# Kernel optimization log

Measured on AMD Instinct MI355X. Metric: run time of the kernel, lower is better.

## Reference

```python
import jax, jax.numpy as jnp
import numpy as np
import math

V, D, NHEAD, NHID, NLAYERS = 50258, 1024, 8, 2048, 2
NUIDS, B, S, TOPK = 2000, 4, 256, 20


def layer_norm(x, g, b):
    m = x.mean(-1, keepdims=True)
    v = ((x - m) ** 2).mean(-1, keepdims=True)
    return (x - m) / jnp.sqrt(v + 1e-5) * g + b


def mha(x, Wqkv, bqkv, Wo, bo):
    Bx, Sx, Dx = x.shape
    hd = Dx // NHEAD
    qkv = x @ Wqkv.T + bqkv                       # [B,S,3D]
    q, k, v = jnp.split(qkv, 3, axis=-1)
    q = q.reshape(Bx, Sx, NHEAD, hd)
    k = k.reshape(Bx, Sx, NHEAD, hd)
    v = v.reshape(Bx, Sx, NHEAD, hd)
    att = jnp.einsum('bqhd,bkhd->bhqk', q, k) / math.sqrt(hd)
    att = jax.nn.softmax(att, axis=-1)
    o = jnp.einsum('bhqk,bkhd->bqhd', att, v).reshape(Bx, Sx, Dx)
    return o @ Wo.T + bo


def enc_layer(x, Wqkv, bqkv, Wo, bo, W1, b1, W2, b2, g1, be1, g2, be2):
    # torch TransformerEncoderLayer, post-LN, relu, dropout=0 (eval)
    x = layer_norm(x + mha(x, Wqkv, bqkv, Wo, bo), g1, be1)
    ff = jax.nn.relu(x @ W1.T + b1) @ W2.T + b2
    return layer_norm(x + ff, g2, be2)


def setup_inputs() -> dict:
    key = jax.random.key(0)
    ks = jax.random.split(key, 32)
    s = 0.02
    inp = {
        'inputs': jax.random.randint(ks[0], (B, S), 0, V),
        'uids': jnp.arange(NUIDS),
        'noise': jax.random.normal(ks[1], (NUIDS,), dtype=jnp.float32),
        'responses_hidden': jax.random.normal(ks[2], (B, S, D), dtype=jnp.float32),
        'topk': TOPK,
        'emb': jax.random.normal(ks[3], (V, D), dtype=jnp.float32) * s,
        # routing encoder (1 layer)
        'r_Wqkv': jax.random.normal(ks[4], (3 * D, D)) * s,
        'r_bqkv': jnp.zeros((3 * D,)),
        'r_Wo': jax.random.normal(ks[5], (D, D)) * s,
        'r_bo': jnp.zeros((D,)),
        'r_W1': jax.random.normal(ks[6], (NHID, D)) * s,
        'r_b1': jnp.zeros((NHID,)),
        'r_W2': jax.random.normal(ks[7], (D, NHID)) * s,
        'r_b2': jnp.zeros((D,)),
        'r_ln1g': jnp.ones((D,)), 'r_ln1b': jnp.zeros((D,)),
        'r_ln2g': jnp.ones((D,)), 'r_ln2b': jnp.zeros((D,)),
        # main encoder (NLAYERS, stacked)
        'e_Wqkv': jax.random.normal(ks[8], (NLAYERS, 3 * D, D)) * s,
        'e_bqkv': jnp.zeros((NLAYERS, 3 * D)),
        'e_Wo': jax.random.normal(ks[9], (NLAYERS, D, D)) * s,
        'e_bo': jnp.zeros((NLAYERS, D)),
        'e_W1': jax.random.normal(ks[10], (NLAYERS, NHID, D)) * s,
        'e_b1': jnp.zeros((NLAYERS, NHID)),
        'e_W2': jax.random.normal(ks[11], (NLAYERS, D, NHID)) * s,
        'e_b2': jnp.zeros((NLAYERS, D)),
        'e_ln1g': jnp.ones((NLAYERS, D)), 'e_ln1b': jnp.zeros((NLAYERS, D)),
        'e_ln2g': jnp.ones((NLAYERS, D)), 'e_ln2b': jnp.zeros((NLAYERS, D)),
        'dec_W': jax.random.normal(ks[12], (V, D)) * s,
        # 2000 tiny gates fused into one [NUIDS, D] matmul
        'gate_W': jax.random.normal(ks[13], (NUIDS, D)) * s,
        'gate_b': jnp.zeros((NUIDS,)),
    }
    return inp


def reference(inputs, uids, noise, responses_hidden, topk, emb,
              r_Wqkv, r_bqkv, r_Wo, r_bo, r_W1, r_b1, r_W2, r_b2,
              r_ln1g, r_ln1b, r_ln2g, r_ln2b,
              e_Wqkv, e_bqkv, e_Wo, e_bo, e_W1, e_b1, e_W2, e_b2,
              e_ln1g, e_ln1b, e_ln2g, e_ln2b,
              dec_W, gate_W, gate_b):
    # --- routing path ---
    h = emb[inputs]                                            # [B,S,D]
    rc = enc_layer(h, r_Wqkv, r_bqkv, r_Wo, r_bo, r_W1, r_b1,
                   r_W2, r_b2, r_ln1g, r_ln1b, r_ln2g, r_ln2b)
    rc = rc * math.sqrt(D)
    # fused per-UID gates: 2000 Linear(D,1) -> one [B,NUIDS] matmul
    rw = rc[:, -1, :] @ gate_W.T + gate_b                      # [B,NUIDS]
    bw = rw.mean(axis=0)                                       # [NUIDS]
    noisy = noise * jnp.std(bw)
    full = jnp.zeros((NUIDS,), dtype=bw.dtype).at[uids].set(bw + noisy)
    topk_w, topk_uids = jax.lax.top_k(full, topk)
    # --- target loss on joined responses ---
    x = responses_hidden
    for l in range(NLAYERS):
        x = enc_layer(x, e_Wqkv[l], e_bqkv[l], e_Wo[l], e_bo[l],
                      e_W1[l], e_b1[l], e_W2[l], e_b2[l],
                      e_ln1g[l], e_ln1b[l], e_ln2g[l], e_ln2b[l])
    logits = x @ dec_W.T                                       # [B,S,V]
    shift_logits = logits[:, :-1, :].reshape(-1, V)
    shift_labels = inputs[:, 1:].reshape(-1)
    logp = jax.nn.log_softmax(shift_logits, axis=-1)
    loss = -jnp.take_along_axis(logp, shift_labels[:, None], axis=1).mean()
    return loss, topk_w, topk_uids
```

## Files before the change

kernel.cpp:

```cpp
#include <hip/hip_runtime.h>

typedef unsigned short ushort_t;
typedef __bf16 bf16x8_t __attribute__((ext_vector_type(8)));
typedef float f32x4_t __attribute__((ext_vector_type(4)));

#define AS1(p) ((const __attribute__((address_space(1))) void*)(p))
#define AS3(p) ((__attribute__((address_space(3))) void*)(p))
#define DEVINL __device__ __forceinline__

DEVINL ushort_t f2bf(float f) {
    unsigned int u = __builtin_bit_cast(unsigned int, f);
    u += 0x7fffu + ((u >> 16) & 1u);
    return (ushort_t)(u >> 16);
}
DEVINL float bf2f(ushort_t h) {
    unsigned int u = ((unsigned int)h) << 16;
    return __builtin_bit_cast(float, u);
}

DEVINL float warp_sum(float v) {
#pragma unroll
    for (int o = 32; o > 0; o >>= 1) v += __shfl_xor(v, o);
    return v;
}
DEVINL float warp_max(float v) {
#pragma unroll
    for (int o = 32; o > 0; o >>= 1) v = fmaxf(v, __shfl_xor(v, o));
    return v;
}
DEVINL float block_sum(float v, float* sb) {
    v = warp_sum(v);
    int w = threadIdx.x >> 6;
    if ((threadIdx.x & 63) == 0) sb[w] = v;
    __syncthreads();
    v = sb[0] + sb[1] + sb[2] + sb[3];
    __syncthreads();
    return v;
}
DEVINL float block_max(float v, float* sb) {
    v = warp_max(v);
    int w = threadIdx.x >> 6;
    if ((threadIdx.x & 63) == 0) sb[w] = v;
    __syncthreads();
    v = fmaxf(fmaxf(sb[0], sb[1]), fmaxf(sb[2], sb[3]));
    __syncthreads();
    return v;
}

template <int EPI>
__global__ __launch_bounds__(256) void gemm_bt(
    const ushort_t* __restrict__ A, long lda, long sA1, long sA2,
    const ushort_t* __restrict__ B, long ldb, long sB1, long sB2,
    void* __restrict__ Cp, long ldc, long sC1, long sC2,
    const float* __restrict__ bias, int accum,
    int K, int batch2, int n_real,
    const int* __restrict__ labels,
    float* __restrict__ part_m, float* __restrict__ part_s,
    float* __restrict__ label_logit)
{
    __shared__ __align__(16) __bf16 As[128 * 32];
    __shared__ __align__(16) __bf16 Bs[128 * 32];

    const int tid = threadIdx.x;
    const int lane = tid & 63;
    const int wave = tid >> 6;
    const int wm = wave >> 1, wn = wave & 1;
    const int quad = lane >> 4, l16 = lane & 15;
    const long m0 = (long)blockIdx.y * 128;
    const long n0 = (long)blockIdx.x * 128;
    const int z = blockIdx.z;
    const int z1 = z / batch2, z2 = z % batch2;
    A += (long)z1 * sA1 + (long)z2 * sA2;
    B += (long)z1 * sB1 + (long)z2 * sB2;

    f32x4_t acc[4][4];
#pragma unroll
    for (int i = 0; i < 4; i++)
#pragma unroll
        for (int j = 0; j < 4; j++) {
            f32x4_t zv = {0.f, 0.f, 0.f, 0.f};
            acc[i][j] = zv;
        }

    const int ea = tid * 8;
    const int nkt = K >> 5;
    for (int kt = 0; kt < nkt; ++kt) {
        const int k0 = kt << 5;
#pragma unroll
        for (int inst = 0; inst < 2; ++inst) {
            int e = ea + inst * 2048;
            int row = e >> 5, kk = e & 31;
            const ushort_t* ga = A + (m0 + row) * lda + k0 + kk;
            const ushort_t* gb = B + (n0 + row) * ldb + k0 + kk;
            __builtin_amdgcn_global_load_lds(AS1(ga), AS3(As + e), 16, 0, 0);
            __builtin_amdgcn_global_load_lds(AS1(gb), AS3(Bs + e), 16, 0, 0);
        }
        __syncthreads();
        bf16x8_t af[4], bfr[4];
#pragma unroll
        for (int i = 0; i < 4; i++)
            af[i] = *(const bf16x8_t*)(As + (wm * 64 + i * 16 + l16) * 32 + quad * 8);
#pragma unroll
        for (int j = 0; j < 4; j++)
            bfr[j] = *(const bf16x8_t*)(Bs + (wn * 64 + j * 16 + l16) * 32 + quad * 8);
#pragma unroll
        for (int i = 0; i < 4; i++)
#pragma unroll
            for (int j = 0; j < 4; j++)
                acc[i][j] = __builtin_amdgcn_mfma_f32_16x16x32_bf16(af[i], bfr[j], acc[i][j], 0, 0, 0);
        __syncthreads();
    }

    if constexpr (EPI == 3) {
#pragma unroll
        for (int i = 0; i < 4; i++) {
#pragma unroll
            for (int reg = 0; reg < 4; reg++) {
                long row = m0 + wm * 64 + i * 16 + quad * 4 + reg;
                int lab = labels[row];
                float mx = -INFINITY;
#pragma unroll
                for (int j = 0; j < 4; j++) {
                    long col = n0 + wn * 64 + j * 16 + l16;
                    float v = acc[i][j][reg];
                    if (col < n_real) mx = fmaxf(mx, v);
                }
#pragma unroll
                for (int o = 8; o > 0; o >>= 1) mx = fmaxf(mx, __shfl_xor(mx, o));
                float sm = 0.f;
#pragma unroll
                for (int j = 0; j < 4; j++) {
                    long col = n0 + wn * 64 + j * 16 + l16;
                    float v = acc[i][j][reg];
                    if (col < n_real) sm += __expf(v - mx);
                    if (col == lab) label_logit[row] = v;
                }
#pragma unroll
                for (int o = 8; o > 0; o >>= 1) sm += __shfl_xor(sm, o);
                if (l16 == 0) {
                    long pidx = row * 786 + (long)blockIdx.x * 2 + wn;
                    part_m[pidx] = mx;
                    part_s[pidx] = sm;
                }
            }
        }
    } else if constexpr (EPI == 0) {
        float* C = (float*)Cp + (long)z1 * sC1 + (long)z2 * sC2;
#pragma unroll
        for (int i = 0; i < 4; i++)
#pragma unroll
            for (int reg = 0; reg < 4; reg++) {
                long row = m0 + wm * 64 + i * 16 + quad * 4 + reg;
#pragma unroll
                for (int j = 0; j < 4; j++) {
                    long col = n0 + wn * 64 + j * 16 + l16;
                    float v = acc[i][j][reg];
                    if (bias) v += bias[col];
                    long idx = row * ldc + col;
                    if (accum) v += C[idx];
                    C[idx] = v;
                }
            }
    } else {
        ushort_t* C = (ushort_t*)Cp + (long)z1 * sC1 + (long)z2 * sC2;
#pragma unroll
        for (int i = 0; i < 4; i++)
#pragma unroll
            for (int reg = 0; reg < 4; reg++) {
                long row = m0 + wm * 64 + i * 16 + quad * 4 + reg;
#pragma unroll
                for (int j = 0; j < 4; j++) {
                    long col = n0 + wn * 64 + j * 16 + l16;
                    float v = acc[i][j][reg];
                    if (bias) v += bias[col];
                    if constexpr (EPI == 2) v = fmaxf(v, 0.f);
                    C[row * ldc + col] = f2bf(v);
                }
            }
    }
}


__global__ __launch_bounds__(256) void k_convert(const float* __restrict__ src,
                                                 ushort_t* __restrict__ dst, long n) {
    long i = ((long)blockIdx.x * 256 + threadIdx.x) * 4;
    if (i >= n) return;
    float4 v = *(const float4*)(src + i);
    dst[i + 0] = f2bf(v.x); dst[i + 1] = f2bf(v.y);
    dst[i + 2] = f2bf(v.z); dst[i + 3] = f2bf(v.w);
}

__global__ __launch_bounds__(256) void k_convert_pad(const float* __restrict__ src,
                                                     ushort_t* __restrict__ dst,
                                                     long n_src, long n_dst) {
    long i = ((long)blockIdx.x * 256 + threadIdx.x) * 4;
    if (i >= n_dst) return;
    if (i < n_src) {
        float4 v = *(const float4*)(src + i);
        dst[i + 0] = f2bf(v.x); dst[i + 1] = f2bf(v.y);
        dst[i + 2] = f2bf(v.z); dst[i + 3] = f2bf(v.w);
    } else {
        dst[i + 0] = 0; dst[i + 1] = 0; dst[i + 2] = 0; dst[i + 3] = 0;
    }
}

__global__ __launch_bounds__(256) void k_convert2(const float* __restrict__ src,
                                                  ushort_t* __restrict__ hi,
                                                  ushort_t* __restrict__ lo, long n) {
    long i = ((long)blockIdx.x * 256 + threadIdx.x) * 4;
    if (i >= n) return;
    float4 v = *(const float4*)(src + i);
    float vv[4] = {v.x, v.y, v.z, v.w};
#pragma unroll
    for (int j = 0; j < 4; j++) {
        ushort_t h = f2bf(vv[j]);
        hi[i + j] = h;
        lo[i + j] = f2bf(vv[j] - bf2f(h));
    }
}

__global__ __launch_bounds__(256) void k_gather2(const int* __restrict__ inputs,
                                                 const float* __restrict__ emb,
                                                 ushort_t* __restrict__ hi,
                                                 ushort_t* __restrict__ lo) {
    int t = blockIdx.x, tid = threadIdx.x;
    long row = inputs[t];
    float4 v = *(const float4*)(emb + row * 1024 + tid * 4);
    long base = (long)t * 1024 + tid * 4;
    float vv[4] = {v.x, v.y, v.z, v.w};
#pragma unroll
    for (int j = 0; j < 4; j++) {
        ushort_t h = f2bf(vv[j]);
        hi[base + j] = h;
        lo[base + j] = f2bf(vv[j] - bf2f(h));
    }
}

__global__ __launch_bounds__(256) void k_rattn(const float* __restrict__ rqkv,
                                               float* __restrict__ o_rt) {
    int zz = blockIdx.x, b = zz >> 3, h = zz & 7, tid = threadIdx.x;
    __shared__ __align__(16) float q[128];
    __shared__ float p[256];
    __shared__ float sb[8];
    const float* base = rqkv + (long)b * 786432 + h * 128;
    if (tid < 128) q[tid] = base[(long)255 * 3072 + tid];
    __syncthreads();
    const float4* q4 = (const float4*)q;
    const float4* kr = (const float4*)(base + 1024 + (long)tid * 3072);
    float a = 0.f;
#pragma unroll 8
    for (int k = 0; k < 32; k++) {
        float4 wv = kr[k], xv = q4[k];
        a += wv.x * xv.x + wv.y * xv.y + wv.z * xv.z + wv.w * xv.w;
    }
    a *= 0.08838834764831845f;
    float m = block_max(a, sb);
    float e = __expf(a - m);
    float ssum = block_sum(e, sb);
    p[tid] = e / ssum;
    __syncthreads();
    if (tid < 128) {
        float acc = 0.f;
        const float* vb = base + 2048 + tid;
        for (int s = 0; s < 256; s++) acc += p[s] * vb[(long)s * 3072];
        o_rt[b * 1024 + h * 128 + tid] = acc;
    }
}

__global__ __launch_bounds__(256) void k_rwo(
    const float* __restrict__ o_rt, const int* __restrict__ inputs,
    const float* __restrict__ emb, const float* __restrict__ Wo,
    const float* __restrict__ bo, float* __restrict__ rbuf)
{
    __shared__ __align__(16) float xs[4096];
    int tid = threadIdx.x;
#pragma unroll
    for (int i = 0; i < 16; i++) xs[i * 256 + tid] = o_rt[i * 256 + tid];
    __syncthreads();
    int wave = tid >> 6, lane = tid & 63;
    int d = blockIdx.x * 4 + wave;
    const float4* wr = (const float4*)(Wo + (long)d * 1024) + lane * 4;
    const float4* x0 = (const float4*)xs + lane * 4;
    const float4* x1 = (const float4*)(xs + 1024) + lane * 4;
    const float4* x2 = (const float4*)(xs + 2048) + lane * 4;
    const float4* x3 = (const float4*)(xs + 3072) + lane * 4;
    float a0 = 0, a1 = 0, a2 = 0, a3 = 0;
#pragma unroll
    for (int k = 0; k < 4; k++) {
        float4 w = wr[k];
        float4 v0 = x0[k], v1 = x1[k], v2 = x2[k], v3 = x3[k];
        a0 += w.x * v0.x + w.y * v0.y + w.z * v0.z + w.w * v0.w;
        a1 += w.x * v1.x + w.y * v1.y + w.z * v1.z + w.w * v1.w;
        a2 += w.x * v2.x + w.y * v2.y + w.z * v2.z + w.w * v2.w;
        a3 += w.x * v3.x + w.y * v3.y + w.z * v3.z + w.w * v3.w;
    }
    a0 = warp_sum(a0); a1 = warp_sum(a1); a2 = warp_sum(a2); a3 = warp_sum(a3);
    if (lane < 4) {
        float a = (lane == 0) ? a0 : (lane == 1) ? a1 : (lane == 2) ? a2 : a3;
        long tok = inputs[lane * 256 + 255];
        rbuf[lane * 1024 + d] = emb[tok * 1024 + d] + bo[d] + a;
    }
}

__global__ __launch_bounds__(256) void k_rln(const float* __restrict__ r,
                                             const float* __restrict__ g,
                                             const float* __restrict__ be,
                                             float* __restrict__ outp, float scale) {
    int row = blockIdx.x, tid = threadIdx.x;
    __shared__ float sb[8];
    const float* rr = r + (long)row * 1024;
    float v[4], s = 0.f, sq = 0.f;
#pragma unroll
    for (int i = 0; i < 4; i++) {
        v[i] = rr[i * 256 + tid];
        s += v[i]; sq += v[i] * v[i];
    }
    s = block_sum(s, sb); sq = block_sum(sq, sb + 4);
    float mean = s * (1.f / 1024.f);
    float rstd = rsqrtf(sq * (1.f / 1024.f) - mean * mean + 1e-5f);
#pragma unroll
    for (int i = 0; i < 4; i++) {
        int d = i * 256 + tid;
        outp[(long)row * 1024 + d] = ((v[i] - mean) * rstd * g[d] + be[d]) * scale;
    }
}

__global__ __launch_bounds__(256) void k_rff1(
    const float* __restrict__ x1f, const float* __restrict__ W1,
    const float* __restrict__ b1, float* __restrict__ f1f)
{
    __shared__ __align__(16) float xs[4096];
    int tid = threadIdx.x;
#pragma unroll
    for (int i = 0; i < 16; i++) xs[i * 256 + tid] = x1f[i * 256 + tid];
    __syncthreads();
    int wave = tid >> 6, lane = tid & 63;
    int j = blockIdx.x * 4 + wave;
    const float4* wr = (const float4*)(W1 + (long)j * 1024) + lane * 4;
    const float4* x0 = (const float4*)xs + lane * 4;
    const float4* x1 = (const float4*)(xs + 1024) + lane * 4;
    const float4* x2 = (const float4*)(xs + 2048) + lane * 4;
    const float4* x3 = (const float4*)(xs + 3072) + lane * 4;
    float a0 = 0, a1 = 0, a2 = 0, a3 = 0;
#pragma unroll
    for (int k = 0; k < 4; k++) {
        float4 w = wr[k];
        float4 v0 = x0[k], v1 = x1[k], v2 = x2[k], v3 = x3[k];
        a0 += w.x * v0.x + w.y * v0.y + w.z * v0.z + w.w * v0.w;
        a1 += w.x * v1.x + w.y * v1.y + w.z * v1.z + w.w * v1.w;
        a2 += w.x * v2.x + w.y * v2.y + w.z * v2.z + w.w * v2.w;
        a3 += w.x * v3.x + w.y * v3.y + w.z * v3.z + w.w * v3.w;
    }
    a0 = warp_sum(a0); a1 = warp_sum(a1); a2 = warp_sum(a2); a3 = warp_sum(a3);
    if (lane < 4) {
        float a = (lane == 0) ? a0 : (lane == 1) ? a1 : (lane == 2) ? a2 : a3;
        f1f[lane * 2048 + j] = fmaxf(b1[j] + a, 0.f);
    }
}

__global__ __launch_bounds__(256) void k_rff2(
    const float* __restrict__ f1f, const float* __restrict__ x1f,
    const float* __restrict__ W2, const float* __restrict__ b2,
    float* __restrict__ r2f)
{
    __shared__ __align__(16) float xs[8192];
    int tid = threadIdx.x;
#pragma unroll
    for (int i = 0; i < 32; i++) xs[i * 256 + tid] = f1f[i * 256 + tid];
    __syncthreads();
    int wave = tid >> 6, lane = tid & 63;
    int d = blockIdx.x * 4 + wave;
    const float4* wr = (const float4*)(W2 + (long)d * 2048) + lane * 8;
    const float4* x0 = (const float4*)xs + lane * 8;
    const float4* x1 = (const float4*)(xs + 2048) + lane * 8;
    const float4* x2 = (const float4*)(xs + 4096) + lane * 8;
    const float4* x3 = (const float4*)(xs + 6144) + lane * 8;
    float a0 = 0, a1 = 0, a2 = 0, a3 = 0;
#pragma unroll
    for (int k = 0; k < 8; k++) {
        float4 w = wr[k];
        float4 v0 = x0[k], v1 = x1[k], v2 = x2[k], v3 = x3[k];
        a0 += w.x * v0.x + w.y * v0.y + w.z * v0.z + w.w * v0.w;
        a1 += w.x * v1.x + w.y * v1.y + w.z * v1.z + w.w * v1.w;
        a2 += w.x * v2.x + w.y * v2.y + w.z * v2.z + w.w * v2.w;
        a3 += w.x * v3.x + w.y * v3.y + w.z * v3.z + w.w * v3.w;
    }
    a0 = warp_sum(a0); a1 = warp_sum(a1); a2 = warp_sum(a2); a3 = warp_sum(a3);
    if (lane < 4) {
        float a = (lane == 0) ? a0 : (lane == 1) ? a1 : (lane == 2) ? a2 : a3;
        r2f[lane * 1024 + d] = x1f[lane * 1024 + d] + b2[d] + a;
    }
}

__global__ __launch_bounds__(256) void k_gate(const float* __restrict__ rc,
                                              const float* __restrict__ gw,
                                              const float* __restrict__ gb,
                                              float* __restrict__ bw) {
    __shared__ __align__(16) float xs[4096];
    int tid = threadIdx.x;
#pragma unroll
    for (int i = 0; i < 16; i++) xs[i * 256 + tid] = rc[i * 256 + tid];
    __syncthreads();
    int wave = tid >> 6, lane = tid & 63;
    int u = blockIdx.x * 4 + wave;
    const float4* wr = (const float4*)(gw + (long)u * 1024) + lane * 4;
    const float4* x0 = (const float4*)xs + lane * 4;
    const float4* x1 = (const float4*)(xs + 1024) + lane * 4;
    const float4* x2 = (const float4*)(xs + 2048) + lane * 4;
    const float4* x3 = (const float4*)(xs + 3072) + lane * 4;
    float a0 = 0, a1 = 0, a2 = 0, a3 = 0;
#pragma unroll
    for (int k = 0; k < 4; k++) {
        float4 w = wr[k];
        float4 v0 = x0[k], v1 = x1[k], v2 = x2[k], v3 = x3[k];
        a0 += w.x * v0.x + w.y * v0.y + w.z * v0.z + w.w * v0.w;
        a1 += w.x * v1.x + w.y * v1.y + w.z * v1.z + w.w * v1.w;
        a2 += w.x * v2.x + w.y * v2.y + w.z * v2.z + w.w * v2.w;
        a3 += w.x * v3.x + w.y * v3.y + w.z * v3.z + w.w * v3.w;
    }
    a0 = warp_sum(a0); a1 = warp_sum(a1); a2 = warp_sum(a2); a3 = warp_sum(a3);
    if (lane == 0)
        bw[u] = 0.25f * (a0 + a1 + a2 + a3) + gb[u];
}

__global__ __launch_bounds__(256) void k_topk(const float* __restrict__ bw,
                                              const int* __restrict__ uids,
                                              const float* __restrict__ noise,
                                              float* __restrict__ out) {
    int tid = threadIdx.x;
    __shared__ float full[2000];
    __shared__ float sb[8];
    __shared__ float rv[256];
    __shared__ int ri[256];
    float s = 0.f, sq = 0.f;
    for (int u = tid; u < 2000; u += 256) {
        float v = bw[u];
        s += v; sq += v * v;
    }
    s = block_sum(s, sb); sq = block_sum(sq, sb + 4);
    float mean = s * (1.f / 2000.f);
    float sd = sqrtf(fmaxf(sq * (1.f / 2000.f) - mean * mean, 0.f));
    for (int i = tid; i < 2000; i += 256) full[i] = 0.f;
    __syncthreads();
    for (int i = tid; i < 2000; i += 256) {
        int u = uids[i];
        if (u >= 0 && u < 2000) full[u] = bw[i] + noise[i] * sd;
    }
    __syncthreads();
    for (int it = 0; it < 20; ++it) {
        float bv = -INFINITY;
        int bi = 0x7fffffff;
        for (int i = tid; i < 2000; i += 256) {
            float v = full[i];
            if (v > bv || (v == bv && i < bi)) { bv = v; bi = i; }
        }
        rv[tid] = bv; ri[tid] = bi;
        __syncthreads();
        for (int stride = 128; stride > 0; stride >>= 1) {
            if (tid < stride) {
                float v2 = rv[tid + stride]; int i2 = ri[tid + stride];
                if (v2 > rv[tid] || (v2 == rv[tid] && i2 < ri[tid])) { rv[tid] = v2; ri[tid] = i2; }
            }
            __syncthreads();
        }
        if (tid == 0) {
            out[1 + it] = rv[0];
            out[21 + it] = (float)ri[0];
            full[ri[0]] = -INFINITY;
        }
        __syncthreads();
    }
}

__global__ __launch_bounds__(256) void k_vt(const ushort_t* __restrict__ qkv,
                                            ushort_t* __restrict__ vt) {
    int zz = blockIdx.y, b = zz >> 3, h = zz & 7;
    int s0 = blockIdx.x * 64, tid = threadIdx.x;
    __shared__ ushort_t t[64][130];
#pragma unroll
    for (int r = 0; r < 32; r++) {
        int idx = r * 256 + tid;
        int sl = idx >> 7, d = idx & 127;
        t[sl][d] = qkv[((long)(b * 256 + s0 + sl)) * 3072 + 2048 + h * 128 + d];
    }
    __syncthreads();
#pragma unroll
    for (int r = 0; r < 32; r++) {
        int idx = r * 256 + tid;
        int d = idx >> 6, sl = idx & 63;
        vt[((long)(zz * 128 + d)) * 256 + s0 + sl] = t[sl][d];
    }
}

__global__ void k_softmax(const float* __restrict__ S, ushort_t* __restrict__ P) {
    long row = blockIdx.x;
    int lane = threadIdx.x;
    const float* sr = S + row * 256;
    float v[4];
    float m = -INFINITY;
#pragma unroll
    for (int i = 0; i < 4; i++) {
        v[i] = sr[i * 64 + lane] * 0.08838834764831845f;
        m = fmaxf(m, v[i]);
    }
    m = warp_max(m);
    float s = 0.f;
#pragma unroll
    for (int i = 0; i < 4; i++) { v[i] = __expf(v[i] - m); s += v[i]; }
    s = warp_sum(s);
    float inv = 1.f / s;
#pragma unroll
    for (int i = 0; i < 4; i++) P[row * 256 + i * 64 + lane] = f2bf(v[i] * inv);
}

__global__ __launch_bounds__(256) void k_addln(const float* __restrict__ x,
                                               const float* __restrict__ y,
                                               const float* __restrict__ g,
                                               const float* __restrict__ b,
                                               float* __restrict__ xf,
                                               ushort_t* __restrict__ xb) {
    int row = blockIdx.x, tid = threadIdx.x;
    const float* xr = x + (long)row * 1024;
    const float* yr = y + (long)row * 1024;
    __shared__ float sb[8];
    float r[4], s = 0.f, sq = 0.f;
#pragma unroll
    for (int i = 0; i < 4; i++) {
        int d = i * 256 + tid;
        r[i] = xr[d] + yr[d];
        s += r[i]; sq += r[i] * r[i];
    }
    s = block_sum(s, sb); sq = block_sum(sq, sb + 4);
    float mean = s * (1.f / 1024.f);
    float rstd = rsqrtf(sq * (1.f / 1024.f) - mean * mean + 1e-5f);
#pragma unroll
    for (int i = 0; i < 4; i++) {
        int d = i * 256 + tid;
        float o = (r[i] - mean) * rstd * g[d] + b[d];
        xf[(long)row * 1024 + d] = o;
        xb[(long)row * 1024 + d] = f2bf(o);
    }
}

__global__ __launch_bounds__(256) void k_labels(const int* __restrict__ inputs,
                                                int* __restrict__ labels) {
    int t = blockIdx.x * 256 + threadIdx.x;
    labels[t] = ((t & 255) == 255) ? -1 : inputs[t + 1];
}

__global__ __launch_bounds__(256) void k_ce(const float* __restrict__ pm,
                                            const float* __restrict__ ps,
                                            const float* __restrict__ ll,
                                            const int* __restrict__ labels,
                                            float* __restrict__ rloss) {
    const int NB = 786;
    long row = blockIdx.x;
    int tid = threadIdx.x;
    __shared__ float sb[8];
    float m = -INFINITY;
    for (int i = tid; i < NB; i += 256) m = fmaxf(m, pm[row * NB + i]);
    m = block_max(m, sb);
    float s = 0.f;
    for (int i = tid; i < NB; i += 256) s += ps[row * NB + i] * __expf(pm[row * NB + i] - m);
    s = block_sum(s, sb);
    if (tid == 0) {
        int lab = labels[row];
        rloss[row] = (lab >= 0) ? (m + logf(s) - ll[row]) : 0.f;
    }
}

__global__ __launch_bounds__(256) void k_final(const float* __restrict__ rloss,
                                               float* __restrict__ out) {
    float s = 0.f;
    for (int i = threadIdx.x; i < 1024; i += 256) s += rloss[i];
    __shared__ float sb[8];
    s = block_sum(s, sb);
    if (threadIdx.x == 0) out[0] = s / 1020.0f;
}


extern "C" void kernel_launch(void* const* d_in, const int* in_sizes, int n_in,
                              void* d_out, int out_size, void* d_ws, size_t ws_size,
                              hipStream_t stream) {
    const int* inputs  = (const int*)d_in[0];
    const int* uids    = (const int*)d_in[1];
    const float* noise = (const float*)d_in[2];
    const float* resp  = (const float*)d_in[3];
    const float* emb   = (const float*)d_in[5];
    const float* r_Wqkv = (const float*)d_in[6];
    const float* r_bqkv = (const float*)d_in[7];
    const float* r_Wo = (const float*)d_in[8];
    const float* r_bo = (const float*)d_in[9];
    const float* r_W1 = (const float*)d_in[10];
    const float* r_b1 = (const float*)d_in[11];
    const float* r_W2 = (const float*)d_in[12];
    const float* r_b2 = (const float*)d_in[13];
    const float* r_ln1g = (const float*)d_in[14];
    const float* r_ln1b = (const float*)d_in[15];
    const float* r_ln2g = (const float*)d_in[16];
    const float* r_ln2b = (const float*)d_in[17];
    const float* e_Wqkv = (const float*)d_in[18];
    const float* e_bqkv = (const float*)d_in[19];
    const float* e_Wo = (const float*)d_in[20];
    const float* e_bo = (const float*)d_in[21];
    const float* e_W1 = (const float*)d_in[22];
    const float* e_b1 = (const float*)d_in[23];
    const float* e_W2 = (const float*)d_in[24];
    const float* e_b2 = (const float*)d_in[25];
    const float* e_ln1g = (const float*)d_in[26];
    const float* e_ln1b = (const float*)d_in[27];
    const float* e_ln2g = (const float*)d_in[28];
    const float* e_ln2b = (const float*)d_in[29];
    const float* dec_W = (const float*)d_in[30];
    const float* gate_W = (const float*)d_in[31];
    const float* gate_b = (const float*)d_in[32];
    float* out = (float*)d_out;
    (void)in_sizes; (void)n_in; (void)out_size; (void)ws_size;

    char* wp = (char*)d_ws;
    auto alloc = [&](size_t bytes) {
        char* p = wp;
        wp += (bytes + 255) & ~(size_t)255;
        return p;
    };
    ushort_t* wqr_hi = (ushort_t*)alloc(3145728ull * 2);
    ushort_t* wqr_lo = (ushort_t*)alloc(3145728ull * 2);
    ushort_t* wq_e = (ushort_t*)alloc(6291456ull * 2);
    ushort_t* wo_e = (ushort_t*)alloc(2097152ull * 2);
    ushort_t* w1_e = (ushort_t*)alloc(4194304ull * 2);
    ushort_t* w2_e = (ushort_t*)alloc(4194304ull * 2);
    ushort_t* decb = (ushort_t*)alloc(51511296ull * 2);
    ushort_t* h_hi = (ushort_t*)alloc(1048576ull * 2);
    ushort_t* h_lo = (ushort_t*)alloc(1048576ull * 2);
    float* rqkv = (float*)alloc(3145728ull * 4);
    float* o_rt = (float*)alloc(4096ull * 4);
    float* rbuf = (float*)alloc(4096ull * 4);
    float* x1f = (float*)alloc(4096ull * 4);
    float* f1f = (float*)alloc(8192ull * 4);
    float* r2f = (float*)alloc(4096ull * 4);
    float* rc = (float*)alloc(4096ull * 4);
    float* bw = (float*)alloc(2000ull * 4);
    ushort_t* xb = (ushort_t*)alloc(1048576ull * 2);
    float* xf = (float*)alloc(1048576ull * 4);
    ushort_t* qkvb = (ushort_t*)alloc(3145728ull * 2);
    ushort_t* vt = (ushort_t*)alloc(1048576ull * 2);
    float* Sb = (float*)alloc(2097152ull * 4);
    ushort_t* Pb = (ushort_t*)alloc(2097152ull * 2);
    ushort_t* ob = (ushort_t*)alloc(1048576ull * 2);
    float* tmpf = (float*)alloc(1048576ull * 4);
    ushort_t* ff1b = (ushort_t*)alloc(2097152ull * 2);
    float* pm = (float*)alloc(1024ull * 786 * 4);
    float* ps = (float*)alloc(1024ull * 786 * 4);
    float* ll = (float*)alloc(1024ull * 4);
    int* labels = (int*)alloc(1024ull * 4);
    float* rloss = (float*)alloc(1024ull * 4);

    auto gemm = [&](int epi, const ushort_t* A_, long lda_, long sA1_, long sA2_,
                    const ushort_t* B_, long ldb_, long sB1_, long sB2_,
                    void* C_, long ldc_, long sC1_, long sC2_,
                    const float* bias_, int accum_, int M_, int N_, int K_,
                    int batch_, int batch2_, int n_real_, const int* labels_,
                    float* pm_, float* ps_, float* ll_) {
        dim3 g((unsigned)(N_ / 128), (unsigned)(M_ / 128), (unsigned)batch_);
        switch (epi) {
        case 0: gemm_bt<0><<<g, 256, 0, stream>>>(A_, lda_, sA1_, sA2_, B_, ldb_, sB1_, sB2_, C_, ldc_, sC1_, sC2_, bias_, accum_, K_, batch2_, n_real_, labels_, pm_, ps_, ll_); break;
        case 1: gemm_bt<1><<<g, 256, 0, stream>>>(A_, lda_, sA1_, sA2_, B_, ldb_, sB1_, sB2_, C_, ldc_, sC1_, sC2_, bias_, accum_, K_, batch2_, n_real_, labels_, pm_, ps_, ll_); break;
        case 2: gemm_bt<2><<<g, 256, 0, stream>>>(A_, lda_, sA1_, sA2_, B_, ldb_, sB1_, sB2_, C_, ldc_, sC1_, sC2_, bias_, accum_, K_, batch2_, n_real_, labels_, pm_, ps_, ll_); break;
        case 3: gemm_bt<3><<<g, 256, 0, stream>>>(A_, lda_, sA1_, sA2_, B_, ldb_, sB1_, sB2_, C_, ldc_, sC1_, sC2_, bias_, accum_, K_, batch2_, n_real_, labels_, pm_, ps_, ll_); break;
        }
    };

    k_convert2<<<3072, 256, 0, stream>>>(r_Wqkv, wqr_hi, wqr_lo, 3145728L);
    k_convert<<<6144, 256, 0, stream>>>(e_Wqkv, wq_e, 6291456L);
    k_convert<<<2048, 256, 0, stream>>>(e_Wo, wo_e, 2097152L);
    k_convert<<<4096, 256, 0, stream>>>(e_W1, w1_e, 4194304L);
    k_convert<<<4096, 256, 0, stream>>>(e_W2, w2_e, 4194304L);
    k_convert_pad<<<50304, 256, 0, stream>>>(dec_W, decb, 51464192L, 51511296L);
    k_convert<<<1024, 256, 0, stream>>>(resp, xb, 1048576L);
    k_gather2<<<1024, 256, 0, stream>>>(inputs, emb, h_hi, h_lo);

    gemm(0, h_hi, 1024, 0, 0, wqr_hi, 1024, 0, 0, rqkv, 3072, 0, 0, r_bqkv, 0, 1024, 3072, 1024, 1, 1, 0, nullptr, nullptr, nullptr, nullptr);
    gemm(0, h_hi, 1024, 0, 0, wqr_lo, 1024, 0, 0, rqkv, 3072, 0, 0, nullptr, 1, 1024, 3072, 1024, 1, 1, 0, nullptr, nullptr, nullptr, nullptr);
    gemm(0, h_lo, 1024, 0, 0, wqr_hi, 1024, 0, 0, rqkv, 3072, 0, 0, nullptr, 1, 1024, 3072, 1024, 1, 1, 0, nullptr, nullptr, nullptr, nullptr);
    k_rattn<<<32, 256, 0, stream>>>(rqkv, o_rt);
    k_rwo<<<256, 256, 0, stream>>>(o_rt, inputs, emb, r_Wo, r_bo, rbuf);
    k_rln<<<4, 256, 0, stream>>>(rbuf, r_ln1g, r_ln1b, x1f, 1.0f);
    k_rff1<<<512, 256, 0, stream>>>(x1f, r_W1, r_b1, f1f);
    k_rff2<<<256, 256, 0, stream>>>(f1f, x1f, r_W2, r_b2, r2f);
    k_rln<<<4, 256, 0, stream>>>(r2f, r_ln2g, r_ln2b, rc, 32.0f);
    k_gate<<<500, 256, 0, stream>>>(rc, gate_W, gate_b, bw);
    k_topk<<<1, 256, 0, stream>>>(bw, uids, noise, out);

    for (int l = 0; l < 2; ++l) {
        gemm(1, xb, 1024, 0, 0, wq_e + (size_t)l * 3145728, 1024, 0, 0, qkvb, 3072, 0, 0,
             e_bqkv + l * 3072, 0, 1024, 3072, 1024, 1, 1, 0, nullptr, nullptr, nullptr, nullptr);
        k_vt<<<dim3(4, 32), 256, 0, stream>>>(qkvb, vt);
        gemm(0, qkvb, 3072, 786432, 128, qkvb + 1024, 3072, 786432, 128, Sb, 256, 524288, 65536,
             nullptr, 0, 256, 256, 128, 32, 8, 0, nullptr, nullptr, nullptr, nullptr);
        k_softmax<<<8192, 64, 0, stream>>>(Sb, Pb);
        gemm(1, Pb, 256, 524288, 65536, vt, 256, 262144, 32768, ob, 1024, 262144, 128,
             nullptr, 0, 256, 128, 256, 32, 8, 0, nullptr, nullptr, nullptr, nullptr);
        gemm(0, ob, 1024, 0, 0, wo_e + (size_t)l * 1048576, 1024, 0, 0, tmpf, 1024, 0, 0,
             e_bo + l * 1024, 0, 1024, 1024, 1024, 1, 1, 0, nullptr, nullptr, nullptr, nullptr);
        k_addln<<<1024, 256, 0, stream>>>((l == 0) ? resp : (const float*)xf, tmpf,
                                          e_ln1g + l * 1024, e_ln1b + l * 1024, xf, xb);
        gemm(2, xb, 1024, 0, 0, w1_e + (size_t)l * 2097152, 1024, 0, 0, ff1b, 2048, 0, 0,
             e_b1 + l * 2048, 0, 1024, 2048, 1024, 1, 1, 0, nullptr, nullptr, nullptr, nullptr);
        gemm(0, ff1b, 2048, 0, 0, w2_e + (size_t)l * 2097152, 2048, 0, 0, tmpf, 1024, 0, 0,
             e_b2 + l * 1024, 0, 1024, 1024, 2048, 1, 1, 0, nullptr, nullptr, nullptr, nullptr);
        k_addln<<<1024, 256, 0, stream>>>(xf, tmpf, e_ln2g + l * 1024, e_ln2b + l * 1024, xf, xb);
    }

    k_labels<<<4, 256, 0, stream>>>(inputs, labels);
    gemm(3, xb, 1024, 0, 0, decb, 1024, 0, 0, nullptr, 0, 0, 0,
         nullptr, 0, 1024, 50304, 1024, 1, 1, 50258, labels, pm, ps, ll);
    k_ce<<<1024, 256, 0, stream>>>(pm, ps, ll, labels, rloss);
    k_final<<<1, 256, 0, stream>>>(rloss, out);
}
```

Measured before the change: 1.345 ms.

## Fuse routing split-precision GEMMs, compute only last-token query, retile decoder CE GEMM

```diff
diff --git a/kernel.cpp b/kernel.cpp
--- a/kernel.cpp
+++ b/kernel.cpp
@@ -52,11 +52,7 @@
     const ushort_t* __restrict__ A, long lda, long sA1, long sA2,
     const ushort_t* __restrict__ B, long ldb, long sB1, long sB2,
     void* __restrict__ Cp, long ldc, long sC1, long sC2,
-    const float* __restrict__ bias, int accum,
-    int K, int batch2, int n_real,
-    const int* __restrict__ labels,
-    float* __restrict__ part_m, float* __restrict__ part_s,
-    float* __restrict__ label_logit)
+    const float* __restrict__ bias, int accum, int K, int batch2)
 {
     __shared__ __align__(16) __bf16 As[128 * 32];
     __shared__ __align__(16) __bf16 Bs[128 * 32];
@@ -90,10 +86,8 @@
         for (int inst = 0; inst < 2; ++inst) {
             int e = ea + inst * 2048;
             int row = e >> 5, kk = e & 31;
-            const ushort_t* ga = A + (m0 + row) * lda + k0 + kk;
-            const ushort_t* gb = B + (n0 + row) * ldb + k0 + kk;
-            __builtin_amdgcn_global_load_lds(AS1(ga), AS3(As + e), 16, 0, 0);
-            __builtin_amdgcn_global_load_lds(AS1(gb), AS3(Bs + e), 16, 0, 0);
+            __builtin_amdgcn_global_load_lds(AS1(A + (m0 + row) * lda + k0 + kk), AS3(As + e), 16, 0, 0);
+            __builtin_amdgcn_global_load_lds(AS1(B + (n0 + row) * ldb + k0 + kk), AS3(Bs + e), 16, 0, 0);
         }
         __syncthreads();
         bf16x8_t af[4], bfr[4];
@@ -111,40 +105,7 @@
         __syncthreads();
     }
 
-    if constexpr (EPI == 3) {
-#pragma unroll
-        for (int i = 0; i < 4; i++) {
-#pragma unroll
-            for (int reg = 0; reg < 4; reg++) {
-                long row = m0 + wm * 64 + i * 16 + quad * 4 + reg;
-                int lab = labels[row];
-                float mx = -INFINITY;
-#pragma unroll
-                for (int j = 0; j < 4; j++) {
-                    long col = n0 + wn * 64 + j * 16 + l16;
-                    float v = acc[i][j][reg];
-                    if (col < n_real) mx = fmaxf(mx, v);
-                }
-#pragma unroll
-                for (int o = 8; o > 0; o >>= 1) mx = fmaxf(mx, __shfl_xor(mx, o));
-                float sm = 0.f;
-#pragma unroll
-                for (int j = 0; j < 4; j++) {
-                    long col = n0 + wn * 64 + j * 16 + l16;
-                    float v = acc[i][j][reg];
-                    if (col < n_real) sm += __expf(v - mx);
-                    if (col == lab) label_logit[row] = v;
-                }
-#pragma unroll
-                for (int o = 8; o > 0; o >>= 1) sm += __shfl_xor(sm, o);
-                if (l16 == 0) {
-                    long pidx = row * 786 + (long)blockIdx.x * 2 + wn;
-                    part_m[pidx] = mx;
-                    part_s[pidx] = sm;
-                }
-            }
-        }
-    } else if constexpr (EPI == 0) {
+    if constexpr (EPI == 0) {
         float* C = (float*)Cp + (long)z1 * sC1 + (long)z2 * sC2;
 #pragma unroll
         for (int i = 0; i < 4; i++)
@@ -180,11 +141,190 @@
     }
 }
 
-
-__global__ __launch_bounds__(256) void k_convert(const float* __restrict__ src,
-                                                 ushort_t* __restrict__ dst, long n) {
+__global__ __launch_bounds__(256) void gemm_split(
+    const ushort_t* __restrict__ Ah, const ushort_t* __restrict__ Al, long lda,
+    const ushort_t* __restrict__ Bh, const ushort_t* __restrict__ Bl, long ldb,
+    float* __restrict__ C, long ldc, const float* __restrict__ bias, int K)
+{
+    __shared__ __align__(16) __bf16 Ahs[4096], Als[4096], Bhs[4096], Bls[4096];
+    const int tid = threadIdx.x;
+    const int lane = tid & 63;
+    const int wave = tid >> 6;
+    const int wm = wave >> 1, wn = wave & 1;
+    const int quad = lane >> 4, l16 = lane & 15;
+    const long m0 = (long)blockIdx.y * 128;
+    const long n0 = (long)blockIdx.x * 128;
+
+    f32x4_t acc[4][4];
+#pragma unroll
+    for (int i = 0; i < 4; i++)
+#pragma unroll
+        for (int j = 0; j < 4; j++) {
+            f32x4_t zv = {0.f, 0.f, 0.f, 0.f};
+            acc[i][j] = zv;
+        }
+
+    const int ea = tid * 8;
+    const int nkt = K >> 5;
+    for (int kt = 0; kt < nkt; ++kt) {
+        const int k0 = kt << 5;
+#pragma unroll
+        for (int inst = 0; inst < 2; ++inst) {
+            int e = ea + inst * 2048;
+            int row = e >> 5, kk = e & 31;
+            long ao = (m0 + row) * lda + k0 + kk;
+            long bo = (n0 + row) * ldb + k0 + kk;
+            __builtin_amdgcn_global_load_lds(AS1(Ah + ao), AS3(Ahs + e), 16, 0, 0);
+            __builtin_amdgcn_global_load_lds(AS1(Al + ao), AS3(Als + e), 16, 0, 0);
+            __builtin_amdgcn_global_load_lds(AS1(Bh + bo), AS3(Bhs + e), 16, 0, 0);
+            __builtin_amdgcn_global_load_lds(AS1(Bl + bo), AS3(Bls + e), 16, 0, 0);
+        }
+        __syncthreads();
+        bf16x8_t ah[4], al[4], bh[4], bl[4];
+#pragma unroll
+        for (int i = 0; i < 4; i++) {
+            int off = (wm * 64 + i * 16 + l16) * 32 + quad * 8;
+            ah[i] = *(const bf16x8_t*)(Ahs + off);
+            al[i] = *(const bf16x8_t*)(Als + off);
+        }
+#pragma unroll
+        for (int j = 0; j < 4; j++) {
+            int off = (wn * 64 + j * 16 + l16) * 32 + quad * 8;
+            bh[j] = *(const bf16x8_t*)(Bhs + off);
+            bl[j] = *(const bf16x8_t*)(Bls + off);
+        }
+#pragma unroll
+        for (int i = 0; i < 4; i++)
+#pragma unroll
+            for (int j = 0; j < 4; j++) {
+                acc[i][j] = __builtin_amdgcn_mfma_f32_16x16x32_bf16(al[i], bh[j], acc[i][j], 0, 0, 0);
+                acc[i][j] = __builtin_amdgcn_mfma_f32_16x16x32_bf16(ah[i], bl[j], acc[i][j], 0, 0, 0);
+                acc[i][j] = __builtin_amdgcn_mfma_f32_16x16x32_bf16(ah[i], bh[j], acc[i][j], 0, 0, 0);
+            }
+        __syncthreads();
+    }
+
+#pragma unroll
+    for (int i = 0; i < 4; i++)
+#pragma unroll
+        for (int reg = 0; reg < 4; reg++) {
+            long row = m0 + wm * 64 + i * 16 + quad * 4 + reg;
+#pragma unroll
+            for (int j = 0; j < 4; j++) {
+                long col = n0 + wn * 64 + j * 16 + l16;
+                C[row * ldc + col] = acc[i][j][reg] + bias[col];
+            }
+        }
+}
+
+__global__ __launch_bounds__(256) void gemm_ce(
+    const ushort_t* __restrict__ A, long lda,
+    const ushort_t* __restrict__ B, long ldb,
+    int K, int n_real, const int* __restrict__ inputs,
+    float* __restrict__ part_m, float* __restrict__ part_s,
+    float* __restrict__ label_logit)
+{
+    __shared__ __align__(16) __bf16 As[256 * 32];
+    __shared__ __align__(16) __bf16 Bs[128 * 32];
+
+    const int tid = threadIdx.x;
+    const int lane = tid & 63;
+    const int wave = tid >> 6;
+    const int quad = lane >> 4, l16 = lane & 15;
+    const long m0 = (long)blockIdx.y * 256;
+    const long n0 = (long)blockIdx.x * 128;
+
+    f32x4_t acc[4][8];
+#pragma unroll
+    for (int i = 0; i < 4; i++)
+#pragma unroll
+        for (int j = 0; j < 8; j++) {
+            f32x4_t zv = {0.f, 0.f, 0.f, 0.f};
+            acc[i][j] = zv;
+        }
+
+    const int ea = tid * 8;
+    const int nkt = K >> 5;
+    for (int kt = 0; kt < nkt; ++kt) {
+        const int k0 = kt << 5;
+#pragma unroll
+        for (int inst = 0; inst < 4; ++inst) {
+            int e = ea + inst * 2048;
+            int row = e >> 5, kk = e & 31;
+            __builtin_amdgcn_global_load_lds(AS1(A + (m0 + row) * lda + k0 + kk), AS3(As + e), 16, 0, 0);
+        }
+#pragma unroll
+        for (int inst = 0; inst < 2; ++inst) {
+            int e = ea + inst * 2048;
+            int row = e >> 5, kk = e & 31;
+            __builtin_amdgcn_global_load_lds(AS1(B + (n0 + row) * ldb + k0 + kk), AS3(Bs + e), 16, 0, 0);
+        }
+        __syncthreads();
+        bf16x8_t af[4], bfr[8];
+#pragma unroll
+        for (int i = 0; i < 4; i++)
+            af[i] = *(const bf16x8_t*)(As + (wave * 64 + i * 16 + l16) * 32 + quad * 8);
+#pragma unroll
+        for (int j = 0; j < 8; j++)
+            bfr[j] = *(const bf16x8_t*)(Bs + (j * 16 + l16) * 32 + quad * 8);
+#pragma unroll
+        for (int i = 0; i < 4; i++)
+#pragma unroll
+            for (int j = 0; j < 8; j++)
+                acc[i][j] = __builtin_amdgcn_mfma_f32_16x16x32_bf16(af[i], bfr[j], acc[i][j], 0, 0, 0);
+        __syncthreads();
+    }
+
+#pragma unroll
+    for (int i = 0; i < 4; i++) {
+#pragma unroll
+        for (int reg = 0; reg < 4; reg++) {
+            long row = m0 + wave * 64 + i * 16 + quad * 4 + reg;
+            int lab = ((row & 255) == 255) ? -1 : inputs[row + 1];
+            float mx = -INFINITY;
+#pragma unroll
+            for (int j = 0; j < 8; j++) {
+                long col = n0 + j * 16 + l16;
+                float v = acc[i][j][reg];
+                if (col < n_real) mx = fmaxf(mx, v);
+            }
+#pragma unroll
+            for (int o = 8; o > 0; o >>= 1) mx = fmaxf(mx, __shfl_xor(mx, o));
+            float sm = 0.f;
+#pragma unroll
+            for (int j = 0; j < 8; j++) {
+                long col = n0 + j * 16 + l16;
+                float v = acc[i][j][reg];
+                if (col < n_real) sm += __expf(v - mx);
+                if (col == lab) label_logit[row] = v;
+            }
+#pragma unroll
+            for (int o = 8; o > 0; o >>= 1) sm += __shfl_xor(sm, o);
+            if (l16 == 0) {
+                long pidx = row * 393 + blockIdx.x;
+                part_m[pidx] = mx;
+                part_s[pidx] = sm;
+            }
+        }
+    }
+}
+
+
+__global__ __launch_bounds__(256) void k_convert_seg(
+    const float* __restrict__ s0, ushort_t* __restrict__ d0, long n0,
+    const float* __restrict__ s1, ushort_t* __restrict__ d1, long n1,
+    const float* __restrict__ s2, ushort_t* __restrict__ d2, long n2,
+    const float* __restrict__ s3, ushort_t* __restrict__ d3, long n3,
+    const float* __restrict__ s4, ushort_t* __restrict__ d4, long n4)
+{
     long i = ((long)blockIdx.x * 256 + threadIdx.x) * 4;
-    if (i >= n) return;
+    const float* src; ushort_t* dst;
+    if (i < n0) { src = s0; dst = d0; }
+    else if ((i -= n0) < n1) { src = s1; dst = d1; }
+    else if ((i -= n1) < n2) { src = s2; dst = d2; }
+    else if ((i -= n2) < n3) { src = s3; dst = d3; }
+    else if ((i -= n3) < n4) { src = s4; dst = d4; }
+    else return;
     float4 v = *(const float4*)(src + i);
     dst[i + 0] = f2bf(v.x); dst[i + 1] = f2bf(v.y);
     dst[i + 2] = f2bf(v.z); dst[i + 3] = f2bf(v.w);
@@ -222,8 +362,10 @@
 __global__ __launch_bounds__(256) void k_gather2(const int* __restrict__ inputs,
                                                  const float* __restrict__ emb,
                                                  ushort_t* __restrict__ hi,
-                                                 ushort_t* __restrict__ lo) {
+                                                 ushort_t* __restrict__ lo,
+                                                 float* __restrict__ loss_out) {
     int t = blockIdx.x, tid = threadIdx.x;
+    if (t == 0 && tid == 0) loss_out[0] = 0.f;
     long row = inputs[t];
     float4 v = *(const float4*)(emb + row * 1024 + tid * 4);
     long base = (long)t * 1024 + tid * 4;
@@ -236,17 +378,54 @@
     }
 }
 
-__global__ __launch_bounds__(256) void k_rattn(const float* __restrict__ rqkv,
+__global__ __launch_bounds__(256) void k_rq(
+    const int* __restrict__ inputs, const float* __restrict__ emb,
+    const float* __restrict__ Wq, const float* __restrict__ bq,
+    float* __restrict__ qf)
+{
+    __shared__ __align__(16) float xs[4096];
+    int tid = threadIdx.x;
+#pragma unroll
+    for (int b2 = 0; b2 < 4; b2++) {
+        long tok = inputs[b2 * 256 + 255];
+        *(float4*)(xs + b2 * 1024 + tid * 4) = *(const float4*)(emb + tok * 1024 + tid * 4);
+    }
+    __syncthreads();
+    int wave = tid >> 6, lane = tid & 63;
+    int d = blockIdx.x * 4 + wave;
+    const float4* wr = (const float4*)(Wq + (long)d * 1024) + lane * 4;
+    const float4* x0 = (const float4*)xs + lane * 4;
+    const float4* x1 = (const float4*)(xs + 1024) + lane * 4;
+    const float4* x2 = (const float4*)(xs + 2048) + lane * 4;
+    const float4* x3 = (const float4*)(xs + 3072) + lane * 4;
+    float a0 = 0, a1 = 0, a2 = 0, a3 = 0;
+#pragma unroll
+    for (int k = 0; k < 4; k++) {
+        float4 w = wr[k];
+        float4 v0 = x0[k], v1 = x1[k], v2 = x2[k], v3 = x3[k];
+        a0 += w.x * v0.x + w.y * v0.y + w.z * v0.z + w.w * v0.w;
+        a1 += w.x * v1.x + w.y * v1.y + w.z * v1.z + w.w * v1.w;
+        a2 += w.x * v2.x + w.y * v2.y + w.z * v2.z + w.w * v2.w;
+        a3 += w.x * v3.x + w.y * v3.y + w.z * v3.z + w.w * v3.w;
+    }
+    a0 = warp_sum(a0); a1 = warp_sum(a1); a2 = warp_sum(a2); a3 = warp_sum(a3);
+    if (lane < 4) {
+        float a = (lane == 0) ? a0 : (lane == 1) ? a1 : (lane == 2) ? a2 : a3;
+        qf[lane * 1024 + d] = a + bq[d];
+    }
+}
+
+__global__ __launch_bounds__(256) void k_rattn(const float* __restrict__ qf,
+                                               const float* __restrict__ kv,
                                                float* __restrict__ o_rt) {
     int zz = blockIdx.x, b = zz >> 3, h = zz & 7, tid = threadIdx.x;
     __shared__ __align__(16) float q[128];
     __shared__ float p[256];
     __shared__ float sb[8];
-    const float* base = rqkv + (long)b * 786432 + h * 128;
-    if (tid < 128) q[tid] = base[(long)255 * 3072 + tid];
+    if (tid < 128) q[tid] = qf[b * 1024 + h * 128 + tid];
     __syncthreads();
     const float4* q4 = (const float4*)q;
-    const float4* kr = (const float4*)(base + 1024 + (long)tid * 3072);
+    const float4* kr = (const float4*)(kv + ((long)(b * 256 + tid)) * 2048 + h * 128);
     float a = 0.f;
 #pragma unroll 8
     for (int k = 0; k < 32; k++) {
@@ -261,8 +440,8 @@
     __syncthreads();
     if (tid < 128) {
         float acc = 0.f;
-        const float* vb = base + 2048 + tid;
-        for (int s = 0; s < 256; s++) acc += p[s] * vb[(long)s * 3072];
+        const float* vb = kv + (long)b * 256 * 2048 + 1024 + h * 128 + tid;
+        for (int s = 0; s < 256; s++) acc += p[s] * vb[(long)s * 2048];
         o_rt[b * 1024 + h * 128 + tid] = acc;
     }
 }
@@ -542,18 +721,12 @@
     }
 }
 
-__global__ __launch_bounds__(256) void k_labels(const int* __restrict__ inputs,
-                                                int* __restrict__ labels) {
-    int t = blockIdx.x * 256 + threadIdx.x;
-    labels[t] = ((t & 255) == 255) ? -1 : inputs[t + 1];
-}
-
 __global__ __launch_bounds__(256) void k_ce(const float* __restrict__ pm,
                                             const float* __restrict__ ps,
                                             const float* __restrict__ ll,
-                                            const int* __restrict__ labels,
-                                            float* __restrict__ rloss) {
-    const int NB = 786;
+                                            const int* __restrict__ inputs,
+                                            float* __restrict__ out) {
+    const int NB = 393;
     long row = blockIdx.x;
     int tid = threadIdx.x;
     __shared__ float sb[8];
@@ -564,18 +737,9 @@
     for (int i = tid; i < NB; i += 256) s += ps[row * NB + i] * __expf(pm[row * NB + i] - m);
     s = block_sum(s, sb);
     if (tid == 0) {
-        int lab = labels[row];
-        rloss[row] = (lab >= 0) ? (m + logf(s) - ll[row]) : 0.f;
-    }
-}
-
-__global__ __launch_bounds__(256) void k_final(const float* __restrict__ rloss,
-                                               float* __restrict__ out) {
-    float s = 0.f;
-    for (int i = threadIdx.x; i < 1024; i += 256) s += rloss[i];
-    __shared__ float sb[8];
-    s = block_sum(s, sb);
-    if (threadIdx.x == 0) out[0] = s / 1020.0f;
+        int lab = ((row & 255) == 255) ? -1 : inputs[row + 1];
+        if (lab >= 0) atomicAdd(out, (m + logf(s) - ll[row]) * (1.0f / 1020.0f));
+    }
 }
 
 
@@ -623,8 +787,8 @@
         wp += (bytes + 255) & ~(size_t)255;
         return p;
     };
-    ushort_t* wqr_hi = (ushort_t*)alloc(3145728ull * 2);
-    ushort_t* wqr_lo = (ushort_t*)alloc(3145728ull * 2);
+    ushort_t* wkv_hi = (ushort_t*)alloc(2097152ull * 2);
+    ushort_t* wkv_lo = (ushort_t*)alloc(2097152ull * 2);
     ushort_t* wq_e = (ushort_t*)alloc(6291456ull * 2);
     ushort_t* wo_e = (ushort_t*)alloc(2097152ull * 2);
     ushort_t* w1_e = (ushort_t*)alloc(4194304ull * 2);
@@ -632,7 +796,8 @@
     ushort_t* decb = (ushort_t*)alloc(51511296ull * 2);
     ushort_t* h_hi = (ushort_t*)alloc(1048576ull * 2);
     ushort_t* h_lo = (ushort_t*)alloc(1048576ull * 2);
-    float* rqkv = (float*)alloc(3145728ull * 4);
+    float* qf = (float*)alloc(4096ull * 4);
+    float* rkv = (float*)alloc(2097152ull * 4);
     float* o_rt = (float*)alloc(4096ull * 4);
     float* rbuf = (float*)alloc(4096ull * 4);
     float* x1f = (float*)alloc(4096ull * 4);
@@ -649,40 +814,37 @@
     ushort_t* ob = (ushort_t*)alloc(1048576ull * 2);
     float* tmpf = (float*)alloc(1048576ull * 4);
     ushort_t* ff1b = (ushort_t*)alloc(2097152ull * 2);
-    float* pm = (float*)alloc(1024ull * 786 * 4);
-    float* ps = (float*)alloc(1024ull * 786 * 4);
+    float* pm = (float*)alloc(1024ull * 393 * 4);
+    float* ps = (float*)alloc(1024ull * 393 * 4);
     float* ll = (float*)alloc(1024ull * 4);
-    int* labels = (int*)alloc(1024ull * 4);
-    float* rloss = (float*)alloc(1024ull * 4);
 
     auto gemm = [&](int epi, const ushort_t* A_, long lda_, long sA1_, long sA2_,
                     const ushort_t* B_, long ldb_, long sB1_, long sB2_,
                     void* C_, long ldc_, long sC1_, long sC2_,
                     const float* bias_, int accum_, int M_, int N_, int K_,
-                    int batch_, int batch2_, int n_real_, const int* labels_,
-                    float* pm_, float* ps_, float* ll_) {
+                    int batch_, int batch2_) {
         dim3 g((unsigned)(N_ / 128), (unsigned)(M_ / 128), (unsigned)batch_);
         switch (epi) {
-        case 0: gemm_bt<0><<<g, 256, 0, stream>>>(A_, lda_, sA1_, sA2_, B_, ldb_, sB1_, sB2_, C_, ldc_, sC1_, sC2_, bias_, accum_, K_, batch2_, n_real_, labels_, pm_, ps_, ll_); break;
-        case 1: gemm_bt<1><<<g, 256, 0, stream>>>(A_, lda_, sA1_, sA2_, B_, ldb_, sB1_, sB2_, C_, ldc_, sC1_, sC2_, bias_, accum_, K_, batch2_, n_real_, labels_, pm_, ps_, ll_); break;
-        case 2: gemm_bt<2><<<g, 256, 0, stream>>>(A_, lda_, sA1_, sA2_, B_, ldb_, sB1_, sB2_, C_, ldc_, sC1_, sC2_, bias_, accum_, K_, batch2_, n_real_, labels_, pm_, ps_, ll_); break;
-        case 3: gemm_bt<3><<<g, 256, 0, stream>>>(A_, lda_, sA1_, sA2_, B_, ldb_, sB1_, sB2_, C_, ldc_, sC1_, sC2_, bias_, accum_, K_, batch2_, n_real_, labels_, pm_, ps_, ll_); break;
+        case 0: gemm_bt<0><<<g, 256, 0, stream>>>(A_, lda_, sA1_, sA2_, B_, ldb_, sB1_, sB2_, C_, ldc_, sC1_, sC2_, bias_, accum_, K_, batch2_); break;
+        case 1: gemm_bt<1><<<g, 256, 0, stream>>>(A_, lda_, sA1_, sA2_, B_, ldb_, sB1_, sB2_, C_, ldc_, sC1_, sC2_, bias_, accum_, K_, batch2_); break;
+        case 2: gemm_bt<2><<<g, 256, 0, stream>>>(A_, lda_, sA1_, sA2_, B_, ldb_, sB1_, sB2_, C_, ldc_, sC1_, sC2_, bias_, accum_, K_, batch2_); break;
         }
     };
 
-    k_convert2<<<3072, 256, 0, stream>>>(r_Wqkv, wqr_hi, wqr_lo, 3145728L);
-    k_convert<<<6144, 256, 0, stream>>>(e_Wqkv, wq_e, 6291456L);
-    k_convert<<<2048, 256, 0, stream>>>(e_Wo, wo_e, 2097152L);
-    k_convert<<<4096, 256, 0, stream>>>(e_W1, w1_e, 4194304L);
-    k_convert<<<4096, 256, 0, stream>>>(e_W2, w2_e, 4194304L);
+    k_convert_seg<<<17408, 256, 0, stream>>>(
+        e_Wqkv, wq_e, 6291456L, e_Wo, wo_e, 2097152L, e_W1, w1_e, 4194304L,
+        e_W2, w2_e, 4194304L, resp, xb, 1048576L);
     k_convert_pad<<<50304, 256, 0, stream>>>(dec_W, decb, 51464192L, 51511296L);
-    k_convert<<<1024, 256, 0, stream>>>(resp, xb, 1048576L);
-    k_gather2<<<1024, 256, 0, stream>>>(inputs, emb, h_hi, h_lo);
-
-    gemm(0, h_hi, 1024, 0, 0, wqr_hi, 1024, 0, 0, rqkv, 3072, 0, 0, r_bqkv, 0, 1024, 3072, 1024, 1, 1, 0, nullptr, nullptr, nullptr, nullptr);
-    gemm(0, h_hi, 1024, 0, 0, wqr_lo, 1024, 0, 0, rqkv, 3072, 0, 0, nullptr, 1, 1024, 3072, 1024, 1, 1, 0, nullptr, nullptr, nullptr, nullptr);
-    gemm(0, h_lo, 1024, 0, 0, wqr_hi, 1024, 0, 0, rqkv, 3072, 0, 0, nullptr, 1, 1024, 3072, 1024, 1, 1, 0, nullptr, nullptr, nullptr, nullptr);
-    k_rattn<<<32, 256, 0, stream>>>(rqkv, o_rt);
+    k_convert2<<<2048, 256, 0, stream>>>(r_Wqkv + 1048576, wkv_hi, wkv_lo, 2097152L);
+    k_gather2<<<1024, 256, 0, stream>>>(inputs, emb, h_hi, h_lo, out);
+
+    k_rq<<<256, 256, 0, stream>>>(inputs, emb, r_Wqkv, r_bqkv, qf);
+    {
+        dim3 g(16, 8);
+        gemm_split<<<g, 256, 0, stream>>>(h_hi, h_lo, 1024, wkv_hi, wkv_lo, 1024,
+                                          rkv, 2048, r_bqkv + 1024, 1024);
+    }
+    k_rattn<<<32, 256, 0, stream>>>(qf, rkv, o_rt);
     k_rwo<<<256, 256, 0, stream>>>(o_rt, inputs, emb, r_Wo, r_bo, rbuf);
     k_rln<<<4, 256, 0, stream>>>(rbuf, r_ln1g, r_ln1b, x1f, 1.0f);
     k_rff1<<<512, 256, 0, stream>>>(x1f, r_W1, r_b1, f1f);
@@ -693,27 +855,27 @@
 
     for (int l = 0; l < 2; ++l) {
         gemm(1, xb, 1024, 0, 0, wq_e + (size_t)l * 3145728, 1024, 0, 0, qkvb, 3072, 0, 0,
-             e_bqkv + l * 3072, 0, 1024, 3072, 1024, 1, 1, 0, nullptr, nullptr, nullptr, nullptr);
+             e_bqkv + l * 3072, 0, 1024, 3072, 1024, 1, 1);
         k_vt<<<dim3(4, 32), 256, 0, stream>>>(qkvb, vt);
         gemm(0, qkvb, 3072, 786432, 128, qkvb + 1024, 3072, 786432, 128, Sb, 256, 524288, 65536,
-             nullptr, 0, 256, 256, 128, 32, 8, 0, nullptr, nullptr, nullptr, nullptr);
+             nullptr, 0, 256, 256, 128, 32, 8);
         k_softmax<<<8192, 64, 0, stream>>>(Sb, Pb);
         gemm(1, Pb, 256, 524288, 65536, vt, 256, 262144, 32768, ob, 1024, 262144, 128,
-             nullptr, 0, 256, 128, 256, 32, 8, 0, nullptr, nullptr, nullptr, nullptr);
+             nullptr, 0, 256, 128, 256, 32, 8);
         gemm(0, ob, 1024, 0, 0, wo_e + (size_t)l * 1048576, 1024, 0, 0, tmpf, 1024, 0, 0,
-             e_bo + l * 1024, 0, 1024, 1024, 1024, 1, 1, 0, nullptr, nullptr, nullptr, nullptr);
+             e_bo + l * 1024, 0, 1024, 1024, 1024, 1, 1);
         k_addln<<<1024, 256, 0, stream>>>((l == 0) ? resp : (const float*)xf, tmpf,
                                           e_ln1g + l * 1024, e_ln1b + l * 1024, xf, xb);
         gemm(2, xb, 1024, 0, 0, w1_e + (size_t)l * 2097152, 1024, 0, 0, ff1b, 2048, 0, 0,
-             e_b1 + l * 2048, 0, 1024, 2048, 1024, 1, 1, 0, nullptr, nullptr, nullptr, nullptr);
+             e_b1 + l * 2048, 0, 1024, 2048, 1024, 1, 1);
         gemm(0, ff1b, 2048, 0, 0, w2_e + (size_t)l * 2097152, 2048, 0, 0, tmpf, 1024, 0, 0,
-             e_b2 + l * 1024, 0, 1024, 1024, 2048, 1, 1, 0, nullptr, nullptr, nullptr, nullptr);
+             e_b2 + l * 1024, 0, 1024, 1024, 2048, 1, 1);
         k_addln<<<1024, 256, 0, stream>>>(xf, tmpf, e_ln2g + l * 1024, e_ln2b + l * 1024, xf, xb);
     }
 
-    k_labels<<<4, 256, 0, stream>>>(inputs, labels);
-    gemm(3, xb, 1024, 0, 0, decb, 1024, 0, 0, nullptr, 0, 0, 0,
-         nullptr, 0, 1024, 50304, 1024, 1, 1, 50258, labels, pm, ps, ll);
-    k_ce<<<1024, 256, 0, stream>>>(pm, ps, ll, labels, rloss);
-    k_final<<<1, 256, 0, stream>>>(rloss, out);
-}
+    {
+        dim3 g(393, 4);
+        gemm_ce<<<g, 256, 0, stream>>>(xb, 1024, decb, 1024, 1024, 50258, inputs, pm, ps, ll);
+    }
+    k_ce<<<1024, 256, 0, stream>>>(pm, ps, ll, inputs, out);
+}
```

New measurement: 1.384 ms. 1.03x slower.
